# Optimization experiments

Hardware: AMD Instinct MI355X
Metric: run time of the kernel (lower is better)

## Reference

```python
import jax, jax.numpy as jnp
import numpy as np

BN_EPS = 1e-5

def conv1x1(x, w, b):
    # x: [B,C,H,W], w: [O,C], b: [O]
    return jnp.einsum('bchw,oc->bohw', x, w) + b[None, :, None, None]

def maxpool2x2(x):
    B, C, H, W = x.shape
    return x.reshape(B, C, H // 2, 2, W // 2, 2).max(axis=(3, 5))

def setup_inputs() -> dict:
    key = jax.random.key(0)
    ks = jax.random.split(key, 11)
    B, C, H, W = 8, 256, 64, 64
    Ci = C // 2  # inter_channels = 128
    s_in = 1.0 / np.sqrt(C)
    s_int = 1.0 / np.sqrt(Ci)
    return {
        'x': jax.random.normal(ks[0], (B, C, H, W), jnp.float32),
        'theta_w': jax.random.uniform(ks[1], (Ci, C), jnp.float32, -s_in, s_in),
        'theta_b': jax.random.uniform(ks[2], (Ci,), jnp.float32, -s_in, s_in),
        'phi_w': jax.random.uniform(ks[3], (Ci, C), jnp.float32, -s_in, s_in),
        'phi_b': jax.random.uniform(ks[4], (Ci,), jnp.float32, -s_in, s_in),
        'g_w': jax.random.uniform(ks[5], (Ci, C), jnp.float32, -s_in, s_in),
        'g_b': jax.random.uniform(ks[6], (Ci,), jnp.float32, -s_in, s_in),
        'W_w': jax.random.uniform(ks[7], (C, Ci), jnp.float32, -s_int, s_int),
        'W_b': jax.random.uniform(ks[8], (C,), jnp.float32, -s_int, s_int),
        'bn_gamma': jax.random.normal(ks[9], (C,), jnp.float32) * 0.1 + 1.0,
        'bn_beta': jax.random.normal(ks[10], (C,), jnp.float32) * 0.1,
    }

def reference(x, theta_w, theta_b, phi_w, phi_b, g_w, g_b, W_w, W_b, bn_gamma, bn_beta):
    B, C, H, W = x.shape
    Ci = theta_w.shape[0]
    # g and phi are sub-sampled (2x2 maxpool) after the 1x1 conv
    g_x = maxpool2x2(conv1x1(x, g_w, g_b)).reshape(B, Ci, -1)        # [B,Ci,M]
    g_x = g_x.transpose(0, 2, 1)                                     # [B,M,Ci]
    theta_x = conv1x1(x, theta_w, theta_b).reshape(B, Ci, -1)        # [B,Ci,N]
    theta_x = theta_x.transpose(0, 2, 1)                             # [B,N,Ci]
    phi_x = maxpool2x2(conv1x1(x, phi_w, phi_b)).reshape(B, Ci, -1)  # [B,Ci,M]
    f = jnp.einsum('bnc,bcm->bnm', theta_x, phi_x)                   # [B,N,M]
    f_div_C = jax.nn.softmax(f, axis=-1)
    y = jnp.einsum('bnm,bmc->bnc', f_div_C, g_x)                     # [B,N,Ci]
    y = y.transpose(0, 2, 1).reshape(B, Ci, H, W)
    # 1x1 conv + BatchNorm2d (training-mode batch statistics)
    W_y = conv1x1(y, W_w, W_b)
    mean = W_y.mean(axis=(0, 2, 3))
    var = W_y.var(axis=(0, 2, 3))
    W_y = (W_y - mean[None, :, None, None]) * jax.lax.rsqrt(var + BN_EPS)[None, :, None, None]
    W_y = W_y * bn_gamma[None, :, None, None] + bn_beta[None, :, None, None]
    return W_y + x
```

## Files before the change

### kernel.cpp

```cpp
#include <hip/hip_runtime.h>
#include <hip/hip_bf16.h>
#include <cstdint>
#include <math.h>

using bf16 = __hip_bfloat16;
typedef __attribute__((ext_vector_type(8))) short bf16x8;
typedef __attribute__((ext_vector_type(4))) float f32x4;

#define DEV __device__ __forceinline__

DEV float b2f(unsigned short u) { return __uint_as_float(((uint32_t)u) << 16); }
DEV float bfl(bf16 h) { return __bfloat162float(h); }
DEV short f2bs(float f) { bf16 h = __float2bfloat16(f); return *(short*)&h; }
DEV uint32_t pk2(float a, float b) {
  return (uint32_t)(unsigned short)f2bs(a) |
         ((uint32_t)(unsigned short)f2bs(b) << 16);
}
DEV float ldv(const void* p, int isbf, int i) {
  return isbf ? bfl(((const bf16*)p)[i]) : ((const float*)p)[i];
}

DEV bf16x8 load_wfrag(const void* w, int isbf, int row, int K, int off) {
  bf16x8 r;
  if (isbf) {
    r = *(const bf16x8*)((const short*)w + (size_t)row * K + off);
  } else {
    const float* f = (const float*)w + (size_t)row * K + off;
    float4 a = *(const float4*)f, b = *(const float4*)(f + 4);
    r[0] = f2bs(a.x); r[1] = f2bs(a.y); r[2] = f2bs(a.z); r[3] = f2bs(a.w);
    r[4] = f2bs(b.x); r[5] = f2bs(b.y); r[6] = f2bs(b.z); r[7] = f2bs(b.w);
  }
  return r;
}

__global__ __launch_bounds__(256) void sniff_kernel(
    const unsigned short* __restrict__ xr, int* __restrict__ flag)
{
  int tid = threadIdx.x;
  int good = 0;
  for (int k = tid; k < 16384; k += 256) {
    unsigned short u = xr[2 * k];
    int e = (u >> 7) & 0xFF;
    good += (e >= 0x6A && e <= 0x86) ? 1 : 0;
  }
  __shared__ int r[256];
  r[tid] = good;
  __syncthreads();
  for (int off = 128; off; off >>= 1) {
    if (tid < off) r[tid] += r[tid + off];
    __syncthreads();
  }
  if (tid == 0) *flag = (r[0] > 9830) ? 1 : 0;
}

__global__ __launch_bounds__(256) void transpose_x(
    const void* __restrict__ x, short* __restrict__ xT, const int* __restrict__ flag)
{
  const int isbf = *flag;
  __shared__ short lt[64 * 71];
  const int n0 = blockIdx.x * 64, c0 = blockIdx.y * 64, b = blockIdx.z;
  const int tid = threadIdx.x;
  for (int it = 0; it < 4; ++it) {
    int idx4 = it * 256 + tid;
    int ci = idx4 >> 4, n4 = (idx4 & 15) * 4;
    size_t go = ((size_t)(b * 256 + c0 + ci)) * 4096 + n0 + n4;
    if (isbf) {
      ushort4 v = *(const ushort4*)((const unsigned short*)x + go);
      lt[ci * 71 + n4 + 0] = v.x; lt[ci * 71 + n4 + 1] = v.y;
      lt[ci * 71 + n4 + 2] = v.z; lt[ci * 71 + n4 + 3] = v.w;
    } else {
      float4 v = *(const float4*)((const float*)x + go);
      lt[ci * 71 + n4 + 0] = f2bs(v.x); lt[ci * 71 + n4 + 1] = f2bs(v.y);
      lt[ci * 71 + n4 + 2] = f2bs(v.z); lt[ci * 71 + n4 + 3] = f2bs(v.w);
    }
  }
  __syncthreads();
  for (int it = 0; it < 4; ++it) {
    int idx4 = it * 256 + tid;
    int n = idx4 >> 4, c4 = (idx4 & 15) * 4;
    ushort4 v;
    v.x = (unsigned short)lt[(c4 + 0) * 71 + n];
    v.y = (unsigned short)lt[(c4 + 1) * 71 + n];
    v.z = (unsigned short)lt[(c4 + 2) * 71 + n];
    v.w = (unsigned short)lt[(c4 + 3) * 71 + n];
    *(ushort4*)(xT + ((size_t)(b * 4096 + n0 + n)) * 256 + c0 + c4) = v;
  }
}

__global__ __launch_bounds__(256) void conv_tp_k(
    const short* __restrict__ xT,
    const void* __restrict__ w1, const void* __restrict__ b1, short* __restrict__ out1,
    const void* __restrict__ w2, const void* __restrict__ b2, short* __restrict__ out2,
    const int* __restrict__ flag)
{
  const int isbf = *flag;
  __shared__ short shA[64 * 264];
  __shared__ short shB[64 * 136];
  const int b = blockIdx.y, nbase = blockIdx.x * 64, tid = threadIdx.x;
  const int ln = tid & 15, q = (tid >> 4) & 3, wv = tid >> 6;
  for (int it = 0; it < 16; ++it) {
    int idx4 = it * 256 + tid;
    int n = idx4 >> 6, c4 = (idx4 & 63) * 4;
    *(ushort4*)&shA[n * 264 + c4] =
        *(const ushort4*)(xT + ((size_t)(b * 4096 + nbase + n)) * 256 + c4);
  }
  __syncthreads();
  f32x4 zero = {0.f, 0.f, 0.f, 0.f};
  f32x4 acc1[4][2], acc2[4][2];
  for (int nt = 0; nt < 4; ++nt)
    for (int ti = 0; ti < 2; ++ti) { acc1[nt][ti] = zero; acc2[nt][ti] = zero; }

  for (int kk = 0; kk < 8; ++kk) {
    int off = kk * 32 + q * 8;
    bf16x8 a[4];
    #pragma unroll
    for (int nt = 0; nt < 4; ++nt)
      a[nt] = *(const bf16x8*)&shA[(16 * nt + ln) * 264 + off];
    #pragma unroll
    for (int ti = 0; ti < 2; ++ti) {
      bf16x8 bw1 = load_wfrag(w1, isbf, 16 * (2 * wv + ti) + ln, 256, off);
      #pragma unroll
      for (int nt = 0; nt < 4; ++nt)
        acc1[nt][ti] = __builtin_amdgcn_mfma_f32_16x16x32_bf16(a[nt], bw1, acc1[nt][ti], 0, 0, 0);
    }
    #pragma unroll
    for (int ti = 0; ti < 2; ++ti) {
      bf16x8 bw2 = load_wfrag(w2, isbf, 16 * (2 * wv + ti) + ln, 256, off);
      #pragma unroll
      for (int nt = 0; nt < 4; ++nt)
        acc2[nt][ti] = __builtin_amdgcn_mfma_f32_16x16x32_bf16(a[nt], bw2, acc2[nt][ti], 0, 0, 0);
    }
  }
  {
    float bv[2];
    for (int ti = 0; ti < 2; ++ti) bv[ti] = ldv(b1, isbf, 16 * (2 * wv + ti) + ln);
    for (int nt = 0; nt < 4; ++nt)
      for (int ti = 0; ti < 2; ++ti)
        for (int r = 0; r < 4; ++r)
          shB[(16 * nt + q * 4 + r) * 136 + 16 * (2 * wv + ti) + ln] =
              f2bs(acc1[nt][ti][r] + bv[ti]);
    __syncthreads();
    for (int it = 0; it < 8; ++it) {
      int idx4 = it * 256 + tid;
      int n = idx4 >> 5, c4 = (idx4 & 31) * 4;
      *(ushort4*)(out1 + ((size_t)(b * 4096 + nbase + n)) * 128 + c4) =
          *(const ushort4*)&shB[n * 136 + c4];
    }
    __syncthreads();
  }
  {
    float bv[2];
    for (int ti = 0; ti < 2; ++ti) bv[ti] = ldv(b2, isbf, 16 * (2 * wv + ti) + ln);
    for (int nt = 0; nt < 4; ++nt)
      for (int ti = 0; ti < 2; ++ti)
        for (int r = 0; r < 4; ++r)
          shB[(16 * nt + q * 4 + r) * 136 + 16 * (2 * wv + ti) + ln] =
              f2bs(acc2[nt][ti][r] + bv[ti]);
    __syncthreads();
    for (int it = 0; it < 8; ++it) {
      int idx4 = it * 256 + tid;
      int n = idx4 >> 5, c4 = (idx4 & 31) * 4;
      *(ushort4*)(out2 + ((size_t)(b * 4096 + nbase + n)) * 128 + c4) =
          *(const ushort4*)&shB[n * 136 + c4];
    }
  }
}

template<int CO, int K>
__global__ __launch_bounds__(256) void conv_n_k(
    const short* __restrict__ inp, const void* __restrict__ w,
    const void* __restrict__ bias, short* __restrict__ out,
    const int* __restrict__ flag)
{
  const int isbf = *flag;
  constexpr int XS = 64 * (K + 8);
  constexpr int OS = CO * 68;
  __shared__ short sh[(XS > OS ? XS : OS)];
  const int b = blockIdx.y, nbase = blockIdx.x * 64, tid = threadIdx.x;
  const int ln = tid & 15, q = (tid >> 4) & 3, wv = tid >> 6;
  constexpr int TPW = CO / 64;
  constexpr int KS = (K == 256) ? 6 : 5;
  for (int it = 0; it < 64 * K / 1024; ++it) {
    int idx4 = it * 256 + tid;
    int n = idx4 >> KS, c4 = (idx4 & ((K / 4) - 1)) * 4;
    *(ushort4*)&sh[n * (K + 8) + c4] =
        *(const ushort4*)(inp + ((size_t)(b * 4096 + nbase + n)) * K + c4);
  }
  __syncthreads();
  f32x4 zero = {0.f, 0.f, 0.f, 0.f};
  f32x4 acc[TPW][4];
  for (int ti = 0; ti < TPW; ++ti) for (int nt = 0; nt < 4; ++nt) acc[ti][nt] = zero;

  for (int kk = 0; kk < K / 32; ++kk) {
    int off = kk * 32 + q * 8;
    bf16x8 bx[4];
    #pragma unroll
    for (int nt = 0; nt < 4; ++nt)
      bx[nt] = *(const bf16x8*)&sh[(16 * nt + ln) * (K + 8) + off];
    #pragma unroll
    for (int ti = 0; ti < TPW; ++ti) {
      bf16x8 aw = load_wfrag(w, isbf, 16 * (TPW * wv + ti) + ln, K, off);
      #pragma unroll
      for (int nt = 0; nt < 4; ++nt)
        acc[ti][nt] = __builtin_amdgcn_mfma_f32_16x16x32_bf16(aw, bx[nt], acc[ti][nt], 0, 0, 0);
    }
  }
  __syncthreads();
  for (int ti = 0; ti < TPW; ++ti)
    for (int r = 0; r < 4; ++r) {
      int co = 16 * (TPW * wv + ti) + q * 4 + r;
      float bb = ldv(bias, isbf, co);
      for (int nt = 0; nt < 4; ++nt)
        sh[co * 68 + 16 * nt + ln] = f2bs(acc[ti][nt][r] + bb);
    }
  __syncthreads();
  for (int it = 0; it < 64 * CO / 1024; ++it) {
    int idx4 = it * 256 + tid;
    int co = idx4 >> 4, n4 = (idx4 & 15) * 4;
    *(ushort4*)(out + ((size_t)(b * CO + co)) * 4096 + nbase + n4) =
        *(const ushort4*)&sh[co * 68 + n4];
  }
}

__global__ __launch_bounds__(256) void pool_phi_kernel(
    const short* __restrict__ pc, short* __restrict__ phi)
{
  int idx = blockIdx.x * 256 + threadIdx.x;
  int ci = idx & 127, m = (idx >> 7) & 1023, b = idx >> 17;
  int mh = m >> 5, mw = m & 31;
  const short* p = pc + ((size_t)(b * 4096 + (mh * 2) * 64 + mw * 2)) * 128 + ci;
  float v = fmaxf(fmaxf(b2f(p[0]), b2f(p[128])),
                  fmaxf(b2f(p[64 * 128]), b2f(p[65 * 128])));
  phi[idx] = f2bs(v);
}

__global__ __launch_bounds__(256) void pool_g_kernel(
    const short* __restrict__ gc, short* __restrict__ g)
{
  int idx = blockIdx.x * 256 + threadIdx.x;
  int m = idx & 1023, bc = idx >> 10;
  int mh = m >> 5, mw = m & 31;
  const short* p = gc + (size_t)bc * 4096 + mh * 128 + mw * 2;
  float v = fmaxf(fmaxf(b2f(p[0]), b2f(p[1])), fmaxf(b2f(p[64]), b2f(p[65])));
  g[idx] = f2bs(v);
}

__global__ __launch_bounds__(256) void attn_kernel(
    const short* __restrict__ theta, const short* __restrict__ phi,
    const short* __restrict__ g, short* __restrict__ y)
{
  __shared__ short ph[64 * 136];
  __shared__ short gl[128 * 72];
  __shared__ short Pl[64 * 72];
  const int b = blockIdx.y, nbase = blockIdx.x * 64, tid = threadIdx.x;
  const int ln = tid & 15, q = (tid >> 4) & 3, wv = tid >> 6;

  const int pm  = tid >> 5;
  const int pc4 = (tid & 31) * 4;
  const int gci = tid >> 4;
  const int gm4 = (tid & 15) * 4;
  const short* phb = phi + (size_t)b * 1024 * 128;
  const short* gb  = g   + (size_t)b * 128 * 1024;

  ushort4 pf_p[8], pf_g[8];
  #pragma unroll
  for (int it = 0; it < 8; ++it)
    pf_p[it] = *(const ushort4*)(phb + ((size_t)(pm + 8 * it)) * 128 + pc4);
  #pragma unroll
  for (int it = 0; it < 8; ++it)
    pf_g[it] = *(const ushort4*)(gb + ((size_t)(gci + 16 * it)) * 1024 + gm4);

  bf16x8 a[4];
  #pragma unroll
  for (int kk = 0; kk < 4; ++kk)
    a[kk] = *(const bf16x8*)(theta +
        ((size_t)(b * 4096 + nbase + 16 * wv + ln)) * 128 + kk * 32 + q * 8);

  f32x4 zero = {0.f, 0.f, 0.f, 0.f};
  f32x4 yacc[8], lacc = zero;
  #pragma unroll
  for (int t = 0; t < 8; ++t) yacc[t] = zero;
  bf16x8 ones;
  #pragma unroll
  for (int j = 0; j < 8; ++j) ones[j] = 0x3F80;

  for (int mc = 0; mc < 16; ++mc) {
    #pragma unroll
    for (int it = 0; it < 8; ++it)
      *(ushort4*)&ph[(pm + 8 * it) * 136 + pc4] = pf_p[it];
    #pragma unroll
    for (int it = 0; it < 8; ++it)
      *(ushort4*)&gl[(gci + 16 * it) * 72 + gm4] = pf_g[it];
    __syncthreads();

    if (mc < 15) {
      const int nmc = mc + 1;
      #pragma unroll
      for (int it = 0; it < 8; ++it)
        pf_p[it] = *(const ushort4*)(phb +
            ((size_t)(nmc * 64 + pm + 8 * it)) * 128 + pc4);
      #pragma unroll
      for (int it = 0; it < 8; ++it)
        pf_g[it] = *(const ushort4*)(gb +
            ((size_t)(gci + 16 * it)) * 1024 + nmc * 64 + gm4);
    }

    #pragma unroll
    for (int t = 0; t < 4; ++t) {
      f32x4 s = zero;
      #pragma unroll
      for (int kk = 0; kk < 4; ++kk) {
        bf16x8 bp = *(const bf16x8*)&ph[(16 * t + ln) * 136 + kk * 32 + q * 8];
        s = __builtin_amdgcn_mfma_f32_16x16x32_bf16(a[kk], bp, s, 0, 0, 0);
      }
      #pragma unroll
      for (int r = 0; r < 4; ++r)
        Pl[(16 * wv + q * 4 + r) * 72 + 16 * t + ln] =
            f2bs(__expf(fminf(s[r], 80.f)));
    }
    bf16x8 ap[2];
    #pragma unroll
    for (int kk = 0; kk < 2; ++kk)
      ap[kk] = *(const bf16x8*)&Pl[(16 * wv + ln) * 72 + kk * 32 + q * 8];
    #pragma unroll
    for (int kk = 0; kk < 2; ++kk)
      lacc = __builtin_amdgcn_mfma_f32_16x16x32_bf16(ap[kk], ones, lacc, 0, 0, 0);
    #pragma unroll
    for (int t = 0; t < 8; ++t) {
      #pragma unroll
      for (int kk = 0; kk < 2; ++kk) {
        bf16x8 bg = *(const bf16x8*)&gl[(16 * t + ln) * 72 + kk * 32 + q * 8];
        yacc[t] = __builtin_amdgcn_mfma_f32_16x16x32_bf16(ap[kk], bg, yacc[t], 0, 0, 0);
      }
    }
    __syncthreads();
  }

  float li[4];
  #pragma unroll
  for (int r = 0; r < 4; ++r) li[r] = 1.0f / lacc[r];
  for (int t = 0; t < 8; ++t)
    for (int r = 0; r < 4; ++r)
      ph[(16 * wv + q * 4 + r) * 136 + 16 * t + ln] = f2bs(yacc[t][r] * li[r]);
  __syncthreads();
  for (int it = 0; it < 8; ++it) {
    int idx4 = it * 256 + tid;
    int n = idx4 >> 5, c4 = (idx4 & 31) * 4;
    *(ushort4*)(y + ((size_t)(b * 4096 + nbase + n)) * 128 + c4) =
        *(const ushort4*)&ph[n * 136 + c4];
  }
}

__global__ __launch_bounds__(256, 4) void convW_k(
    const short* __restrict__ yb, const void* __restrict__ w,
    const void* __restrict__ bias, short* __restrict__ Wy,
    float* __restrict__ stats, const int* __restrict__ flag)
{
  const int isbf = *flag;
  __shared__ short sh[256 * 72];
  const int b = blockIdx.y, nbase = blockIdx.x * 64, tid = threadIdx.x;
  const int ln = tid & 15, q = (tid >> 4) & 3, wv = tid >> 6;

  for (int it = 0; it < 4; ++it) {
    int idx8 = it * 256 + tid;
    int n = idx8 >> 4, c8 = (idx8 & 15) * 8;
    *(uint4*)&sh[n * 136 + c8] =
        *(const uint4*)(yb + ((size_t)(b * 4096 + nbase + n)) * 128 + c8);
  }
  __syncthreads();
  f32x4 zero = {0.f, 0.f, 0.f, 0.f};
  f32x4 acc[4][4];
  for (int ti = 0; ti < 4; ++ti)
    for (int nt = 0; nt < 4; ++nt) acc[ti][nt] = zero;

  for (int kk = 0; kk < 4; ++kk) {
    int off = kk * 32 + q * 8;
    bf16x8 bx[4];
    #pragma unroll
    for (int nt = 0; nt < 4; ++nt)
      bx[nt] = *(const bf16x8*)&sh[(16 * nt + ln) * 136 + off];
    #pragma unroll
    for (int ti = 0; ti < 4; ++ti) {
      bf16x8 aw = load_wfrag(w, isbf, 16 * (4 * wv + ti) + ln, 128, off);
      #pragma unroll
      for (int nt = 0; nt < 4; ++nt)
        acc[ti][nt] = __builtin_amdgcn_mfma_f32_16x16x32_bf16(aw, bx[nt], acc[ti][nt], 0, 0, 0);
    }
  }
  __syncthreads();
  #pragma unroll
  for (int ti = 0; ti < 4; ++ti)
    #pragma unroll
    for (int r = 0; r < 4; ++r) {
      int co = 16 * (4 * wv + ti) + 4 * q + r;
      float bb = ldv(bias, isbf, co);
      #pragma unroll
      for (int nt = 0; nt < 4; ++nt)
        sh[co * 72 + 16 * nt + ln] = f2bs(acc[ti][nt][r] + bb);
    }
  __syncthreads();
  {
    int co = tid;
    float s = 0.f, s2 = 0.f;
    for (int i = 0; i < 64; ++i) {
      float v = b2f((unsigned short)sh[co * 72 + i]);
      s += v; s2 += v * v;
    }
    atomicAdd(&stats[co], s);
    atomicAdd(&stats[256 + co], s2);
  }
  for (int it = 0; it < 8; ++it) {
    int idx8 = it * 256 + tid;
    int co = idx8 >> 3, n8 = (idx8 & 7) * 8;
    *(uint4*)(Wy + ((size_t)(b * 256 + co)) * 4096 + nbase + n8) =
        *(const uint4*)&sh[co * 72 + n8];
  }
}

__global__ __launch_bounds__(256) void bn_apply4(
    const short* __restrict__ Wy, const void* __restrict__ x,
    const float* __restrict__ stats, const void* __restrict__ gamma,
    const void* __restrict__ beta, void* __restrict__ out,
    const int* __restrict__ flag)
{
  const int isbf = *flag;
  int t = blockIdx.x * 256 + threadIdx.x;
  int idx4 = t * 4;
  int c = (idx4 >> 12) & 255;
  float s = stats[c], s2 = stats[256 + c];
  float mean = s * (1.0f / 32768.0f);
  float var = fmaxf(s2 * (1.0f / 32768.0f) - mean * mean, 0.f);
  float scale = rsqrtf(var + 1e-5f) * ldv(gamma, isbf, c);
  float shift = ldv(beta, isbf, c) - mean * scale;
  ushort4 wy = *(const ushort4*)(Wy + idx4);
  float xv[4];
  if (isbf) {
    ushort4 xu = *(const ushort4*)((const unsigned short*)x + idx4);
    xv[0] = b2f(xu.x); xv[1] = b2f(xu.y); xv[2] = b2f(xu.z); xv[3] = b2f(xu.w);
  } else {
    float4 xf = *(const float4*)((const float*)x + idx4);
    xv[0] = xf.x; xv[1] = xf.y; xv[2] = xf.z; xv[3] = xf.w;
  }
  float v0 = b2f(wy.x) * scale + shift + xv[0];
  float v1 = b2f(wy.y) * scale + shift + xv[1];
  float v2 = b2f(wy.z) * scale + shift + xv[2];
  float v3 = b2f(wy.w) * scale + shift + xv[3];
  if (isbf) {
    uint2 o; o.x = pk2(v0, v1); o.y = pk2(v2, v3);
    *(uint2*)((unsigned short*)out + idx4) = o;
  } else {
    float4 o = make_float4(v0, v1, v2, v3);
    *(float4*)((float*)out + idx4) = o;
  }
}

extern "C" void kernel_launch(void* const* d_in, const int* in_sizes, int n_in,
                              void* d_out, int out_size, void* d_ws, size_t ws_size,
                              hipStream_t stream) {
  const void* x       = d_in[0];
  const void* theta_w = d_in[1];
  const void* theta_b = d_in[2];
  const void* phi_w   = d_in[3];
  const void* phi_b   = d_in[4];
  const void* g_w     = d_in[5];
  const void* g_b     = d_in[6];
  const void* W_w     = d_in[7];
  const void* W_b     = d_in[8];
  const void* gamma   = d_in[9];
  const void* beta    = d_in[10];

  char* wsb = (char*)d_ws;
  short* xT      = (short*)(wsb + 0);
  short* ybuf    = (short*)(wsb + 0);
  short* theta   = (short*)(wsb + 16777216);
  short* W_y     = (short*)(wsb + 16777216);
  short* scratch = (short*)(wsb + 25165824);
  short* phi     = (short*)(wsb + 33554432);
  short* gg      = (short*)(wsb + 35651584);
  float* stats   = (float*)(wsb + 37748736);
  int*   flag    = (int*)  (wsb + 37750784);

  dim3 blk(256);
  dim3 cgrid(64, 8);
  dim3 tgrid(64, 4, 8);

  hipMemsetAsync(stats, 0, 2048, stream);
  sniff_kernel<<<1, blk, 0, stream>>>((const unsigned short*)x, flag);
  transpose_x<<<tgrid, blk, 0, stream>>>(x, xT, flag);
  conv_tp_k<<<cgrid, blk, 0, stream>>>(xT, theta_w, theta_b, theta,
                                       phi_w, phi_b, scratch, flag);
  pool_phi_kernel<<<4096, blk, 0, stream>>>(scratch, phi);
  conv_n_k<128, 256><<<cgrid, blk, 0, stream>>>(xT, g_w, g_b, scratch, flag);
  pool_g_kernel<<<4096, blk, 0, stream>>>(scratch, gg);
  attn_kernel<<<cgrid, blk, 0, stream>>>(theta, phi, gg, ybuf);
  convW_k<<<cgrid, blk, 0, stream>>>(ybuf, W_w, W_b, W_y, stats, flag);
  bn_apply4<<<8192, blk, 0, stream>>>(W_y, x, stats, gamma, beta, d_out, flag);
}
```

Measured before the change: 244.6 us.

## Read attention phi/g operands directly from global memory with 512-thread blocks

The attention kernel no longer stages phi and g tiles through shared memory with register prefetch and per-chunk barriers. Each wave now loads its MFMA B operands straight from global memory (expected to hit cache). The block grows to 512 threads covering 128 query rows, and shared memory is kept only for the per-wave P tile and the output transpose. This removes two barriers per chunk and the LDS staging cost, but each wave issues redundant global loads with strided g accesses, and their latency is no longer hidden by prefetch.

```diff
diff --git a/kernel.cpp b/kernel.cpp
--- a/kernel.cpp
+++ b/kernel.cpp
@@ -245,30 +245,15 @@
   g[idx] = f2bs(v);
 }
 
-__global__ __launch_bounds__(256) void attn_kernel(
+__global__ __launch_bounds__(512) void attn_kernel(
     const short* __restrict__ theta, const short* __restrict__ phi,
     const short* __restrict__ g, short* __restrict__ y)
 {
-  __shared__ short ph[64 * 136];
-  __shared__ short gl[128 * 72];
-  __shared__ short Pl[64 * 72];
-  const int b = blockIdx.y, nbase = blockIdx.x * 64, tid = threadIdx.x;
+  __shared__ short sm[128 * 136];
+  const int b = blockIdx.y, nbase = blockIdx.x * 128, tid = threadIdx.x;
   const int ln = tid & 15, q = (tid >> 4) & 3, wv = tid >> 6;
-
-  const int pm  = tid >> 5;
-  const int pc4 = (tid & 31) * 4;
-  const int gci = tid >> 4;
-  const int gm4 = (tid & 15) * 4;
   const short* phb = phi + (size_t)b * 1024 * 128;
   const short* gb  = g   + (size_t)b * 128 * 1024;
-
-  ushort4 pf_p[8], pf_g[8];
-  #pragma unroll
-  for (int it = 0; it < 8; ++it)
-    pf_p[it] = *(const ushort4*)(phb + ((size_t)(pm + 8 * it)) * 128 + pc4);
-  #pragma unroll
-  for (int it = 0; it < 8; ++it)
-    pf_g[it] = *(const ushort4*)(gb + ((size_t)(gci + 16 * it)) * 1024 + gm4);
 
   bf16x8 a[4];
   #pragma unroll
@@ -284,33 +269,16 @@
   #pragma unroll
   for (int j = 0; j < 8; ++j) ones[j] = 0x3F80;
 
+  short* Pl = sm;
+
   for (int mc = 0; mc < 16; ++mc) {
-    #pragma unroll
-    for (int it = 0; it < 8; ++it)
-      *(ushort4*)&ph[(pm + 8 * it) * 136 + pc4] = pf_p[it];
-    #pragma unroll
-    for (int it = 0; it < 8; ++it)
-      *(ushort4*)&gl[(gci + 16 * it) * 72 + gm4] = pf_g[it];
-    __syncthreads();
-
-    if (mc < 15) {
-      const int nmc = mc + 1;
-      #pragma unroll
-      for (int it = 0; it < 8; ++it)
-        pf_p[it] = *(const ushort4*)(phb +
-            ((size_t)(nmc * 64 + pm + 8 * it)) * 128 + pc4);
-      #pragma unroll
-      for (int it = 0; it < 8; ++it)
-        pf_g[it] = *(const ushort4*)(gb +
-            ((size_t)(gci + 16 * it)) * 1024 + nmc * 64 + gm4);
-    }
-
     #pragma unroll
     for (int t = 0; t < 4; ++t) {
       f32x4 s = zero;
       #pragma unroll
       for (int kk = 0; kk < 4; ++kk) {
-        bf16x8 bp = *(const bf16x8*)&ph[(16 * t + ln) * 136 + kk * 32 + q * 8];
+        bf16x8 bp = *(const bf16x8*)(phb +
+            ((size_t)(mc * 64 + 16 * t + ln)) * 128 + kk * 32 + q * 8);
         s = __builtin_amdgcn_mfma_f32_16x16x32_bf16(a[kk], bp, s, 0, 0, 0);
       }
       #pragma unroll
@@ -318,36 +286,34 @@
         Pl[(16 * wv + q * 4 + r) * 72 + 16 * t + ln] =
             f2bs(__expf(fminf(s[r], 80.f)));
     }
-    bf16x8 ap[2];
-    #pragma unroll
-    for (int kk = 0; kk < 2; ++kk)
-      ap[kk] = *(const bf16x8*)&Pl[(16 * wv + ln) * 72 + kk * 32 + q * 8];
-    #pragma unroll
-    for (int kk = 0; kk < 2; ++kk)
-      lacc = __builtin_amdgcn_mfma_f32_16x16x32_bf16(ap[kk], ones, lacc, 0, 0, 0);
+    bf16x8 ap0 = *(const bf16x8*)&Pl[(16 * wv + ln) * 72 + q * 8];
+    bf16x8 ap1 = *(const bf16x8*)&Pl[(16 * wv + ln) * 72 + 32 + q * 8];
+    lacc = __builtin_amdgcn_mfma_f32_16x16x32_bf16(ap0, ones, lacc, 0, 0, 0);
+    lacc = __builtin_amdgcn_mfma_f32_16x16x32_bf16(ap1, ones, lacc, 0, 0, 0);
     #pragma unroll
     for (int t = 0; t < 8; ++t) {
-      #pragma unroll
-      for (int kk = 0; kk < 2; ++kk) {
-        bf16x8 bg = *(const bf16x8*)&gl[(16 * t + ln) * 72 + kk * 32 + q * 8];
-        yacc[t] = __builtin_amdgcn_mfma_f32_16x16x32_bf16(ap[kk], bg, yacc[t], 0, 0, 0);
-      }
-    }
-    __syncthreads();
-  }
+      bf16x8 bg0 = *(const bf16x8*)(gb +
+          ((size_t)(16 * t + ln)) * 1024 + mc * 64 + q * 8);
+      bf16x8 bg1 = *(const bf16x8*)(gb +
+          ((size_t)(16 * t + ln)) * 1024 + mc * 64 + 32 + q * 8);
+      yacc[t] = __builtin_amdgcn_mfma_f32_16x16x32_bf16(ap0, bg0, yacc[t], 0, 0, 0);
+      yacc[t] = __builtin_amdgcn_mfma_f32_16x16x32_bf16(ap1, bg1, yacc[t], 0, 0, 0);
+    }
+  }
+  __syncthreads();
 
   float li[4];
   #pragma unroll
   for (int r = 0; r < 4; ++r) li[r] = 1.0f / lacc[r];
   for (int t = 0; t < 8; ++t)
     for (int r = 0; r < 4; ++r)
-      ph[(16 * wv + q * 4 + r) * 136 + 16 * t + ln] = f2bs(yacc[t][r] * li[r]);
+      sm[(16 * wv + q * 4 + r) * 136 + 16 * t + ln] = f2bs(yacc[t][r] * li[r]);
   __syncthreads();
   for (int it = 0; it < 8; ++it) {
-    int idx4 = it * 256 + tid;
+    int idx4 = it * 512 + tid;
     int n = idx4 >> 5, c4 = (idx4 & 31) * 4;
     *(ushort4*)(y + ((size_t)(b * 4096 + nbase + n)) * 128 + c4) =
-        *(const ushort4*)&ph[n * 136 + c4];
+        *(const ushort4*)&sm[n * 136 + c4];
   }
 }
 
@@ -483,6 +449,7 @@
   dim3 blk(256);
   dim3 cgrid(64, 8);
   dim3 tgrid(64, 4, 8);
+  dim3 agrid(32, 8);
 
   hipMemsetAsync(stats, 0, 2048, stream);
   sniff_kernel<<<1, blk, 0, stream>>>((const unsigned short*)x, flag);
@@ -492,7 +459,7 @@
   pool_phi_kernel<<<4096, blk, 0, stream>>>(scratch, phi);
   conv_n_k<128, 256><<<cgrid, blk, 0, stream>>>(xT, g_w, g_b, scratch, flag);
   pool_g_kernel<<<4096, blk, 0, stream>>>(scratch, gg);
-  attn_kernel<<<cgrid, blk, 0, stream>>>(theta, phi, gg, ybuf);
+  attn_kernel<<<agrid, dim3(512), 0, stream>>>(theta, phi, gg, ybuf);
   convW_k<<<cgrid, blk, 0, stream>>>(ybuf, W_w, W_b, W_y, stats, flag);
   bn_apply4<<<8192, blk, 0, stream>>>(W_y, x, stats, gamma, beta, d_out, flag);
 }
```

Measured after the change: 327.9 us. +34.0%, slower.
